# Kernel tuning notes

Measured on AMD Instinct MI355X. Metric: run time of the kernel, lower is better.

The kernel has to match this reference:

```python
import jax, jax.numpy as jnp
import numpy as np

N_HEADS = 16

def setup_inputs() -> dict:
    key = jax.random.key(0)
    k1, k2, k3 = jax.random.split(key, 3)
    B, L, D = 2, 2048, 1024
    x = jax.random.normal(k1, (B, L, D), dtype=jnp.float32)
    w_qkv = jax.random.normal(k2, (D, 3 * D), dtype=jnp.float32) * (1.0 / np.sqrt(D))
    w_out = jax.random.normal(k3, (D, D), dtype=jnp.float32) * (1.0 / np.sqrt(D))
    return {"x": x, "w_qkv": w_qkv, "w_out": w_out}

def reference(x, w_qkv, w_out):
    B, L, D = x.shape
    H = N_HEADS
    dh = D // H
    qkv = x @ w_qkv                      # (B, L, 3D)
    q, k, v = jnp.split(qkv, 3, axis=-1)
    # (B, H, L, dh)
    q = q.reshape(B, L, H, dh).transpose(0, 2, 1, 3)
    k = k.reshape(B, L, H, dh).transpose(0, 2, 1, 3)
    v = v.reshape(B, L, H, dh).transpose(0, 2, 1, 3)
    scale = 1.0 / jnp.sqrt(jnp.asarray(dh, x.dtype))
    attn = jnp.einsum('bhqd,bhkd->bhqk', q, k) * scale   # (B, H, L, L)
    causal = jnp.tril(jnp.ones((L, L), dtype=bool))
    attn = jnp.where(causal[None, None], attn, -jnp.inf)
    attn = jax.nn.softmax(attn, axis=-1)
    out = jnp.einsum('bhqk,bhkd->bhqd', attn, v)         # (B, H, L, dh)
    out = out.transpose(0, 2, 1, 3).reshape(B, L, D)
    return out @ w_out
```

## Files before the change

### kernel.cpp

```cpp
#include <hip/hip_runtime.h>

typedef __attribute__((ext_vector_type(4))) float f32x4;
typedef __attribute__((ext_vector_type(16))) float f32x16;
typedef __attribute__((ext_vector_type(8))) __bf16 bf16x8;
typedef __attribute__((ext_vector_type(4))) __bf16 bf16x4;
typedef __attribute__((ext_vector_type(4))) unsigned u32x4;
typedef __attribute__((ext_vector_type(2))) unsigned u32x2;

static __device__ __forceinline__ f32x4 mfma16(bf16x8 a, bf16x8 b, f32x4 c) {
    return __builtin_amdgcn_mfma_f32_16x16x32_bf16(a, b, c, 0, 0, 0);
}
static __device__ __forceinline__ f32x16 mfma32(bf16x8 a, bf16x8 b, f32x16 c) {
    return __builtin_amdgcn_mfma_f32_32x32x16_bf16(a, b, c, 0, 0, 0);
}
static __device__ __forceinline__ unsigned pk_bf16(float a, float b) {
    unsigned lo = __builtin_bit_cast(unsigned short, (__bf16)a);
    unsigned hh = __builtin_bit_cast(unsigned short, (__bf16)b);
    return lo | (hh << 16);
}

#define QSCALE 0.18033688f

__global__ __launch_bounds__(256) void cvt_f32_bf16(const float* __restrict__ in,
                                                    __bf16* __restrict__ out, int n4) {
    int i = blockIdx.x * 256 + threadIdx.x;
    if (i < n4) {
        f32x4 v = ((const f32x4*)in)[i];
        bf16x4 o;
#pragma unroll
        for (int j = 0; j < 4; j++) o[j] = (__bf16)v[j];
        ((bf16x4*)out)[i] = o;
    }
}

__global__ __launch_bounds__(256) void transpose_bf16(const float* __restrict__ in,
                                                      __bf16* __restrict__ out,
                                                      int R, int C) {
    __shared__ float t[32][33];
    int bx = blockIdx.x * 32;
    int by = blockIdx.y * 32;
    int tx = threadIdx.x, ty = threadIdx.y;
#pragma unroll
    for (int k = 0; k < 32; k += 8)
        t[ty + k][tx] = in[(size_t)(by + ty + k) * C + bx + tx];
    __syncthreads();
#pragma unroll
    for (int k = 0; k < 32; k += 8)
        out[(size_t)(bx + ty + k) * R + by + tx] = (__bf16)t[tx][ty + k];
}

#define BM 128
#define BN 128
#define BKG 64

template <int MODE>
__global__ __launch_bounds__(256) void gemm_bt(const __bf16* __restrict__ A,
                                               const __bf16* __restrict__ Bt,
                                               int M, int N, int K,
                                               float* __restrict__ Cout,
                                               __bf16* __restrict__ Qf,
                                               __bf16* __restrict__ Kf,
                                               __bf16* __restrict__ Vf) {
    __shared__ __attribute__((aligned(16))) __bf16 As[BM * BKG];
    __shared__ __attribute__((aligned(16))) __bf16 Bs[BN * BKG];
    int tid = threadIdx.x;
    int wave = tid >> 6, lane = tid & 63;
    int lrow = lane & 15, lgrp = lane >> 4;
    int chunk = gridDim.x >> 3;
    int bid = blockIdx.x;
    int swz = (bid & 7) * chunk + (bid >> 3);
    int nbx = N >> 7;
    int m0 = (swz / nbx) * BM, n0 = (swz % nbx) * BN;
    int wm = (wave >> 1) * 64, wn = (wave & 1) * 64;

    f32x4 acc[4][4];
#pragma unroll
    for (int i = 0; i < 4; i++)
#pragma unroll
        for (int j = 0; j < 4; j++) acc[i][j] = (f32x4){0.f, 0.f, 0.f, 0.f};

    int srow = tid >> 3;
    int gch = (tid & 7) ^ (srow & 7);
    const __bf16* aSrc = A + (size_t)(m0 + srow) * K + gch * 8;
    const __bf16* bSrc = Bt + (size_t)(n0 + srow) * K + gch * 8;

    for (int k0 = 0; k0 < K; k0 += BKG) {
#pragma unroll
        for (int c = 0; c < 4; c++) {
            __builtin_amdgcn_global_load_lds(
                (const __attribute__((address_space(1))) void*)(aSrc + k0 + (size_t)c * 32 * K),
                (__attribute__((address_space(3))) void*)(As + (c * 256 + wave * 64) * 8),
                16, 0, 0);
        }
#pragma unroll
        for (int c = 0; c < 4; c++) {
            __builtin_amdgcn_global_load_lds(
                (const __attribute__((address_space(1))) void*)(bSrc + k0 + (size_t)c * 32 * K),
                (__attribute__((address_space(3))) void*)(Bs + (c * 256 + wave * 64) * 8),
                16, 0, 0);
        }
        __syncthreads();
#pragma unroll
        for (int kk = 0; kk < 2; kk++) {
            bf16x8 af[4], bfr[4];
#pragma unroll
            for (int mt = 0; mt < 4; mt++) {
                int row = wm + mt * 16 + lrow;
                int slot = row * 8 + ((4 * kk + lgrp) ^ (row & 7));
                af[mt] = *(const bf16x8*)(As + slot * 8);
            }
#pragma unroll
            for (int nt = 0; nt < 4; nt++) {
                int row = wn + nt * 16 + lrow;
                int slot = row * 8 + ((4 * kk + lgrp) ^ (row & 7));
                bfr[nt] = *(const bf16x8*)(Bs + slot * 8);
            }
#pragma unroll
            for (int mt = 0; mt < 4; mt++)
#pragma unroll
                for (int nt = 0; nt < 4; nt++)
                    acc[mt][nt] = mfma16(af[mt], bfr[nt], acc[mt][nt]);
        }
        __syncthreads();
    }

#pragma unroll
    for (int mt = 0; mt < 4; mt++) {
#pragma unroll
        for (int nt = 0; nt < 4; nt++) {
            int f0 = m0 + wm + mt * 16 + lgrp * 4;
            int t = n0 + wn + nt * 16 + lrow;
            if (MODE == 0) {
                *(f32x4*)(Cout + (size_t)t * M + f0) = acc[mt][nt];
            } else {
                int which = f0 >> 10, hn = f0 & 1023;
                int h = hn >> 6, d0 = hn & 63;
                int b = t >> 11, li = t & 2047;
                int bh = b * 16 + h, c = li >> 5, tl = li & 31;
                size_t bhbase = (size_t)bh * 131072;
                if (which == 2) {
                    int ks = tl >> 4, hv = (tl >> 3) & 1, jv = tl & 7;
                    size_t base =
                        bhbase + ((size_t)(c * 4 + ks * 2 + hv) * 64 + d0) * 8 + jv;
#pragma unroll
                    for (int r = 0; r < 4; r++)
                        Vf[base + (size_t)r * 8] = (__bf16)acc[mt][nt][r];
                } else {
                    int st = d0 >> 4, hv = (d0 >> 3) & 1, j0 = d0 & 7;
                    size_t idx =
                        bhbase + ((size_t)(c * 8 + st * 2 + hv) * 32 + tl) * 8 + j0;
                    bf16x4 pv;
                    if (which == 0) {
#pragma unroll
                        for (int r = 0; r < 4; r++)
                            pv[r] = (__bf16)(acc[mt][nt][r] * QSCALE);
                        *(bf16x4*)(Qf + idx) = pv;
                    } else {
#pragma unroll
                        for (int r = 0; r < 4; r++) pv[r] = (__bf16)acc[mt][nt][r];
                        *(bf16x4*)(Kf + idx) = pv;
                    }
                }
            }
        }
    }
}

template <bool MASKED>
static __device__ __forceinline__ void attn_chunk(
    int c, int ql, int hi, const __bf16* __restrict__ Kp,
    const __bf16* __restrict__ Vp, const bf16x8 (&qf)[4],
    f32x16& o0, f32x16& o1, float& ls) {
    const __bf16* kb = Kp + ((size_t)c * 8 + hi) * 256 + ql * 8;
    bf16x8 kf[4];
#pragma unroll
    for (int st = 0; st < 4; st++) kf[st] = *(const bf16x8*)(kb + st * 512);
    const __bf16* vb = Vp + ((size_t)c * 4 + hi) * 512 + ql * 8;
    bf16x8 v00 = *(const bf16x8*)(vb);
    bf16x8 v01 = *(const bf16x8*)(vb + 256);
    bf16x8 v10 = *(const bf16x8*)(vb + 1024);
    bf16x8 v11 = *(const bf16x8*)(vb + 1280);

    f32x16 sa;
#pragma unroll
    for (int r = 0; r < 16; r++) sa[r] = 0.f;
#pragma unroll
    for (int st = 0; st < 4; st++) sa = mfma32(kf[st], qf[st], sa);

    float p[16];
    float psum = 0.f;
#pragma unroll
    for (int r = 0; r < 16; r++) {
        float s = sa[r];
        if (MASKED) {
            int krel = (r & 3) + 8 * (r >> 2) + 4 * hi;
            if (krel > ql) s = -1e30f;
        }
        float pv = __builtin_amdgcn_exp2f(s);
        p[r] = pv;
        psum += pv;
    }
    u32x2 ps = __builtin_amdgcn_permlane32_swap(
        __builtin_bit_cast(unsigned, psum), __builtin_bit_cast(unsigned, psum),
        false, false);
    psum += __builtin_bit_cast(float, hi ? ps[0] : ps[1]);
    ls += psum;

    unsigned w[8];
#pragma unroll
    for (int i = 0; i < 8; i++) w[i] = pk_bf16(p[2 * i], p[2 * i + 1]);
    u32x2 r02 = __builtin_amdgcn_permlane32_swap(w[0], w[2], false, false);
    u32x2 r13 = __builtin_amdgcn_permlane32_swap(w[1], w[3], false, false);
    u32x2 r46 = __builtin_amdgcn_permlane32_swap(w[4], w[6], false, false);
    u32x2 r57 = __builtin_amdgcn_permlane32_swap(w[5], w[7], false, false);
    bf16x8 pa0 = __builtin_bit_cast(bf16x8, (u32x4){r02[0], r13[0], r02[1], r13[1]});
    bf16x8 pa1 = __builtin_bit_cast(bf16x8, (u32x4){r46[0], r57[0], r46[1], r57[1]});

    o0 = mfma32(pa0, v00, o0);
    o1 = mfma32(pa0, v01, o1);
    o0 = mfma32(pa1, v10, o0);
    o1 = mfma32(pa1, v11, o1);
}

__global__ __launch_bounds__(256) void attn_fwd5(const __bf16* __restrict__ Qf,
                                                 const __bf16* __restrict__ Kf,
                                                 const __bf16* __restrict__ Vf,
                                                 __bf16* __restrict__ Ob) {
    __shared__ float comb[3][64][33];
    int tid = threadIdx.x;
    int wave = tid >> 6, lane = tid & 63;
    int ql = lane & 31, hi = lane >> 5;
    int bid = blockIdx.x;
    int xcd = bid & 7, idx = bid >> 3;
    int bh = xcd * 4 + (idx >> 6);
    int strip = 63 - (idx & 63);
    int q0 = strip * 32;

    const __bf16* Qp = Qf + (size_t)bh * 131072;
    const __bf16* Kp = Kf + (size_t)bh * 131072;
    const __bf16* Vp = Vf + (size_t)bh * 131072;

    const __bf16* qb = Qp + ((size_t)strip * 8 + hi) * 256 + ql * 8;
    bf16x8 qf[4];
#pragma unroll
    for (int st = 0; st < 4; st++) qf[st] = *(const bf16x8*)(qb + st * 512);

    f32x16 o0, o1;
#pragma unroll
    for (int r = 0; r < 16; r++) { o0[r] = 0.f; o1[r] = 0.f; }
    float ls = 0.f;

    for (int c = wave; c < strip; c += 4)
        attn_chunk<false>(c, ql, hi, Kp, Vp, qf, o0, o1, ls);
    if ((strip & 3) == wave)
        attn_chunk<true>(strip, ql, hi, Kp, Vp, qf, o0, o1, ls);

    if (wave >= 1) {
        float* sl = &comb[wave - 1][lane][0];
#pragma unroll
        for (int r = 0; r < 16; r++) { sl[r] = o0[r]; sl[16 + r] = o1[r]; }
        sl[32] = ls;
    }
    __syncthreads();
    if (wave == 0) {
#pragma unroll
        for (int s = 0; s < 3; s++) {
            const float* sl = &comb[s][lane][0];
#pragma unroll
            for (int r = 0; r < 16; r++) { o0[r] += sl[r]; o1[r] += sl[16 + r]; }
            ls += sl[32];
        }
        float inv = 1.0f / ls;
        int b = bh >> 4, h = bh & 15;
#pragma unroll
        for (int r = 0; r < 16; r++) {
            int crow = (r & 3) + 8 * (r >> 2) + 4 * hi;
            float ibc = __shfl(inv, crow);
            size_t base = ((size_t)(b * 2048 + q0 + crow)) * 1024 + h * 64;
            Ob[base + ql] = (__bf16)(o0[r] * ibc);
            Ob[base + 32 + ql] = (__bf16)(o1[r] * ibc);
        }
    }
}

extern "C" void kernel_launch(void* const* d_in, const int* in_sizes, int n_in,
                              void* d_out, int out_size, void* d_ws, size_t ws_size,
                              hipStream_t stream) {
    const float* x = (const float*)d_in[0];
    const float* w_qkv = (const float*)d_in[1];
    const float* w_out = (const float*)d_in[2];
    float* out = (float*)d_out;

    char* ws = (char*)d_ws;
    __bf16* xb    = (__bf16*)(ws);
    __bf16* wqkvT = (__bf16*)(ws + (size_t)(8  << 20));
    __bf16* woutT = (__bf16*)(ws + (size_t)(14 << 20));
    __bf16* Qf    = (__bf16*)(ws + (size_t)(16 << 20));
    __bf16* Kf    = (__bf16*)(ws + (size_t)(24 << 20));
    __bf16* Vf    = (__bf16*)(ws + (size_t)(32 << 20));
    __bf16* Ob    = (__bf16*)(ws + (size_t)(40 << 20));

    cvt_f32_bf16<<<4096, 256, 0, stream>>>(x, xb, 4096 * 1024 / 4);
    transpose_bf16<<<dim3(3072 / 32, 1024 / 32), dim3(32, 8), 0, stream>>>(w_qkv, wqkvT, 1024, 3072);
    transpose_bf16<<<dim3(1024 / 32, 1024 / 32), dim3(32, 8), 0, stream>>>(w_out, woutT, 1024, 1024);
    gemm_bt<1><<<768, 256, 0, stream>>>(
        wqkvT, xb, 3072, 4096, 1024, nullptr, Qf, Kf, Vf);
    attn_fwd5<<<2048, 256, 0, stream>>>(Qf, Kf, Vf, Ob);
    gemm_bt<0><<<256, 256, 0, stream>>>(
        woutT, Ob, 1024, 4096, 1024, out, nullptr, nullptr, nullptr);
}
```

Measured before the change: 110.3 us.

## Replace QKV GEMM with 256x256-tile 8-wave kernel using async LDS loads

```diff
diff --git a/kernel.cpp b/kernel.cpp
--- a/kernel.cpp
+++ b/kernel.cpp
@@ -20,6 +20,13 @@
 }
 
 #define QSCALE 0.18033688f
+#define FENCE() asm volatile("" ::: "memory")
+#define SYNCB()                          \
+    do {                                 \
+        FENCE();                         \
+        __builtin_amdgcn_s_barrier();    \
+        FENCE();                         \
+    } while (0)
 
 __global__ __launch_bounds__(256) void cvt_f32_bf16(const float* __restrict__ in,
                                                     __bf16* __restrict__ out, int n4) {
@@ -49,6 +56,143 @@
         out[(size_t)(bx + ty + k) * R + by + tx] = (__bf16)t[tx][ty + k];
 }
 
+__global__ __launch_bounds__(512, 2) void qkv_gemm8(const __bf16* __restrict__ A,
+                                                    const __bf16* __restrict__ Bt,
+                                                    __bf16* __restrict__ Qf,
+                                                    __bf16* __restrict__ Kf,
+                                                    __bf16* __restrict__ Vf) {
+    const int K = 1024, NT = 16, MT = 12;
+    __shared__ __attribute__((aligned(16))) __bf16 smem[65536];
+    int tid = threadIdx.x;
+    int w = tid >> 6, lane = tid & 63;
+    int lrow = lane & 15, lgrp = lane >> 4;
+    int wm = w >> 2, wn = w & 3;
+    int bid = blockIdx.x;
+    int swz = (bid & 7) * 24 + (bid >> 3);
+    int m0 = (swz % MT) * 256, n0 = (swz / MT) * 256;
+
+    int schunk = ((lane & 3) ^ ((lane >> 2) & 3)) * 8;
+    const __bf16* aS[2];
+    const __bf16* bS[2];
+    int dstRow[2];
+#pragma unroll
+    for (int l = 0; l < 2; l++) {
+        int r = w * 32 + l * 16 + (lane >> 2);
+        aS[l] = A + (size_t)(m0 + r) * K + schunk;
+        bS[l] = Bt + (size_t)(n0 + r) * K + schunk;
+        dstRow[l] = (w * 32 + l * 16) * 64;
+    }
+
+    auto STAGE = [&](int h, int tt) {
+        int tc = tt < NT ? tt : NT - 1;
+        int op = h & 1, kh = h >> 1;
+        int base = ((tt & 1) << 16) + (kh << 15) + (op << 14);
+#pragma unroll
+        for (int l = 0; l < 2; l++) {
+            const __bf16* src = (op ? bS[l] : aS[l]) + tc * 64 + kh * 32;
+            __builtin_amdgcn_global_load_lds(
+                (const __attribute__((address_space(1))) void*)src,
+                (__attribute__((address_space(3))) void*)(smem +
+                                                          ((base + dstRow[l]) >> 1)),
+                16, 0, 0);
+        }
+    };
+
+    int swzsel = (lgrp ^ (lrow & 3)) << 4;
+    auto RDA = [&](int buf, int kk, int row) {
+        int off = (buf << 16) + (kk << 15) + row * 64 + swzsel;
+        return *(const bf16x8*)(smem + (off >> 1));
+    };
+    auto RDB = [&](int buf, int kk, int row) {
+        int off = (buf << 16) + (kk << 15) + 16384 + row * 64 + swzsel;
+        return *(const bf16x8*)(smem + (off >> 1));
+    };
+
+    f32x4 acc[8][4];
+#pragma unroll
+    for (int i = 0; i < 8; i++)
+#pragma unroll
+        for (int j = 0; j < 4; j++) acc[i][j] = (f32x4){0.f, 0.f, 0.f, 0.f};
+    bf16x8 bfr[4];
+
+    STAGE(0, 0); STAGE(1, 0); STAGE(2, 0); STAGE(3, 0);
+    STAGE(0, 1); STAGE(1, 1);
+    asm volatile("s_waitcnt vmcnt(8)" ::: "memory");
+    SYNCB();
+
+#define PH(T, KKv, MHv, SH, ST, DOVM)                                          \
+    {                                                                          \
+        bf16x8 af[4];                                                          \
+        if (MHv == 0) {                                                        \
+            _Pragma("unroll") for (int nt = 0; nt < 4; nt++) bfr[nt] =         \
+                RDB((T) & 1, KKv, wn * 64 + nt * 16 + lrow);                   \
+        }                                                                      \
+        _Pragma("unroll") for (int i = 0; i < 4; i++) af[i] =                  \
+            RDA((T) & 1, KKv, wm * 128 + (MHv * 4 + i) * 16 + lrow);           \
+        STAGE(SH, ST);                                                         \
+        if (DOVM) asm volatile("s_waitcnt vmcnt(8)" ::: "memory");             \
+        SYNCB();                                                               \
+        asm volatile("s_waitcnt lgkmcnt(0)" ::: "memory");                     \
+        __builtin_amdgcn_sched_barrier(0);                                     \
+        __builtin_amdgcn_s_setprio(1);                                         \
+        _Pragma("unroll") for (int i = 0; i < 4; i++)                          \
+            _Pragma("unroll") for (int nt = 0; nt < 4; nt++)                   \
+                acc[MHv * 4 + i][nt] =                                         \
+                    mfma16(af[i], bfr[nt], acc[MHv * 4 + i][nt]);              \
+        __builtin_amdgcn_s_setprio(0);                                         \
+        SYNCB();                                                               \
+    }
+
+#pragma unroll 2
+    for (int t = 0; t < NT; ++t) {
+        PH(t, 0, 0, 2, t + 1, 0);
+        PH(t, 0, 1, 3, t + 1, 1);
+        PH(t, 1, 0, 0, t + 2, 0);
+        PH(t, 1, 1, 1, t + 2, 1);
+    }
+#undef PH
+
+    asm volatile("s_waitcnt vmcnt(0)" ::: "memory");
+    SYNCB();
+
+#pragma unroll
+    for (int mt = 0; mt < 8; mt++) {
+#pragma unroll
+        for (int nt = 0; nt < 4; nt++) {
+            int f0 = m0 + wm * 128 + mt * 16 + lgrp * 4;
+            int t = n0 + wn * 64 + nt * 16 + lrow;
+            int which = f0 >> 10, hn = f0 & 1023;
+            int h = hn >> 6, d0 = hn & 63;
+            int b = t >> 11, li = t & 2047;
+            int bh = b * 16 + h, c = li >> 5, tl = li & 31;
+            size_t bhbase = (size_t)bh * 131072;
+            if (which == 2) {
+                int ks = tl >> 4, hv = (tl >> 3) & 1, jv = tl & 7;
+                size_t base =
+                    bhbase + ((size_t)(c * 4 + ks * 2 + hv) * 64 + d0) * 8 + jv;
+#pragma unroll
+                for (int r = 0; r < 4; r++)
+                    Vf[base + (size_t)r * 8] = (__bf16)acc[mt][nt][r];
+            } else {
+                int st = d0 >> 4, hv = (d0 >> 3) & 1, j0 = d0 & 7;
+                size_t idx =
+                    bhbase + ((size_t)(c * 8 + st * 2 + hv) * 32 + tl) * 8 + j0;
+                bf16x4 pv;
+                if (which == 0) {
+#pragma unroll
+                    for (int r = 0; r < 4; r++)
+                        pv[r] = (__bf16)(acc[mt][nt][r] * QSCALE);
+                    *(bf16x4*)(Qf + idx) = pv;
+                } else {
+#pragma unroll
+                    for (int r = 0; r < 4; r++) pv[r] = (__bf16)acc[mt][nt][r];
+                    *(bf16x4*)(Kf + idx) = pv;
+                }
+            }
+        }
+    }
+}
+
 #define BM 128
 #define BN 128
 #define BKG 64
@@ -57,10 +201,7 @@
 __global__ __launch_bounds__(256) void gemm_bt(const __bf16* __restrict__ A,
                                                const __bf16* __restrict__ Bt,
                                                int M, int N, int K,
-                                               float* __restrict__ Cout,
-                                               __bf16* __restrict__ Qf,
-                                               __bf16* __restrict__ Kf,
-                                               __bf16* __restrict__ Vf) {
+                                               float* __restrict__ Cout) {
     __shared__ __attribute__((aligned(16))) __bf16 As[BM * BKG];
     __shared__ __attribute__((aligned(16))) __bf16 Bs[BN * BKG];
     int tid = threadIdx.x;
@@ -130,38 +271,7 @@
         for (int nt = 0; nt < 4; nt++) {
             int f0 = m0 + wm + mt * 16 + lgrp * 4;
             int t = n0 + wn + nt * 16 + lrow;
-            if (MODE == 0) {
-                *(f32x4*)(Cout + (size_t)t * M + f0) = acc[mt][nt];
-            } else {
-                int which = f0 >> 10, hn = f0 & 1023;
-                int h = hn >> 6, d0 = hn & 63;
-                int b = t >> 11, li = t & 2047;
-                int bh = b * 16 + h, c = li >> 5, tl = li & 31;
-                size_t bhbase = (size_t)bh * 131072;
-                if (which == 2) {
-                    int ks = tl >> 4, hv = (tl >> 3) & 1, jv = tl & 7;
-                    size_t base =
-                        bhbase + ((size_t)(c * 4 + ks * 2 + hv) * 64 + d0) * 8 + jv;
-#pragma unroll
-                    for (int r = 0; r < 4; r++)
-                        Vf[base + (size_t)r * 8] = (__bf16)acc[mt][nt][r];
-                } else {
-                    int st = d0 >> 4, hv = (d0 >> 3) & 1, j0 = d0 & 7;
-                    size_t idx =
-                        bhbase + ((size_t)(c * 8 + st * 2 + hv) * 32 + tl) * 8 + j0;
-                    bf16x4 pv;
-                    if (which == 0) {
-#pragma unroll
-                        for (int r = 0; r < 4; r++)
-                            pv[r] = (__bf16)(acc[mt][nt][r] * QSCALE);
-                        *(bf16x4*)(Qf + idx) = pv;
-                    } else {
-#pragma unroll
-                        for (int r = 0; r < 4; r++) pv[r] = (__bf16)acc[mt][nt][r];
-                        *(bf16x4*)(Kf + idx) = pv;
-                    }
-                }
-            }
+            *(f32x4*)(Cout + (size_t)t * M + f0) = acc[mt][nt];
         }
     }
 }
@@ -303,9 +413,7 @@
     cvt_f32_bf16<<<4096, 256, 0, stream>>>(x, xb, 4096 * 1024 / 4);
     transpose_bf16<<<dim3(3072 / 32, 1024 / 32), dim3(32, 8), 0, stream>>>(w_qkv, wqkvT, 1024, 3072);
     transpose_bf16<<<dim3(1024 / 32, 1024 / 32), dim3(32, 8), 0, stream>>>(w_out, woutT, 1024, 1024);
-    gemm_bt<1><<<768, 256, 0, stream>>>(
-        wqkvT, xb, 3072, 4096, 1024, nullptr, Qf, Kf, Vf);
+    qkv_gemm8<<<192, 512, 0, stream>>>(wqkvT, xb, Qf, Kf, Vf);
     attn_fwd5<<<2048, 256, 0, stream>>>(Qf, Kf, Vf, Ob);
-    gemm_bt<0><<<256, 256, 0, stream>>>(
-        woutT, Ob, 1024, 4096, 1024, out, nullptr, nullptr, nullptr);
-}
+    gemm_bt<0><<<256, 256, 0, stream>>>(woutT, Ob, 1024, 4096, 1024, out);
+}
```

Measured after the change: 110.4 us. About the same (+0.1%).

## Double-buffer GEMM LDS tiles and pair causal attention strips per block

Applied to the files above, without the earlier changes.

```diff
diff --git a/kernel.cpp b/kernel.cpp
--- a/kernel.cpp
+++ b/kernel.cpp
@@ -61,8 +61,8 @@
                                                __bf16* __restrict__ Qf,
                                                __bf16* __restrict__ Kf,
                                                __bf16* __restrict__ Vf) {
-    __shared__ __attribute__((aligned(16))) __bf16 As[BM * BKG];
-    __shared__ __attribute__((aligned(16))) __bf16 Bs[BN * BKG];
+    __shared__ __attribute__((aligned(16))) __bf16 As[2][BM * BKG];
+    __shared__ __attribute__((aligned(16))) __bf16 Bs[2][BN * BKG];
     int tid = threadIdx.x;
     int wave = tid >> 6, lane = tid & 63;
     int lrow = lane & 15, lgrp = lane >> 4;
@@ -84,22 +84,30 @@
     const __bf16* aSrc = A + (size_t)(m0 + srow) * K + gch * 8;
     const __bf16* bSrc = Bt + (size_t)(n0 + srow) * K + gch * 8;
 
-    for (int k0 = 0; k0 < K; k0 += BKG) {
+    auto STAGE = [&](int k0, int b) {
 #pragma unroll
         for (int c = 0; c < 4; c++) {
             __builtin_amdgcn_global_load_lds(
                 (const __attribute__((address_space(1))) void*)(aSrc + k0 + (size_t)c * 32 * K),
-                (__attribute__((address_space(3))) void*)(As + (c * 256 + wave * 64) * 8),
+                (__attribute__((address_space(3))) void*)(As[b] + (c * 256 + wave * 64) * 8),
                 16, 0, 0);
         }
 #pragma unroll
         for (int c = 0; c < 4; c++) {
             __builtin_amdgcn_global_load_lds(
                 (const __attribute__((address_space(1))) void*)(bSrc + k0 + (size_t)c * 32 * K),
-                (__attribute__((address_space(3))) void*)(Bs + (c * 256 + wave * 64) * 8),
+                (__attribute__((address_space(3))) void*)(Bs[b] + (c * 256 + wave * 64) * 8),
                 16, 0, 0);
         }
-        __syncthreads();
+    };
+
+    int nk = K >> 6;
+    STAGE(0, 0);
+    __syncthreads();
+
+    for (int t = 0; t < nk; t++) {
+        int cur = t & 1;
+        if (t + 1 < nk) STAGE((t + 1) << 6, cur ^ 1);
 #pragma unroll
         for (int kk = 0; kk < 2; kk++) {
             bf16x8 af[4], bfr[4];
@@ -107,13 +115,13 @@
             for (int mt = 0; mt < 4; mt++) {
                 int row = wm + mt * 16 + lrow;
                 int slot = row * 8 + ((4 * kk + lgrp) ^ (row & 7));
-                af[mt] = *(const bf16x8*)(As + slot * 8);
+                af[mt] = *(const bf16x8*)(As[cur] + slot * 8);
             }
 #pragma unroll
             for (int nt = 0; nt < 4; nt++) {
                 int row = wn + nt * 16 + lrow;
                 int slot = row * 8 + ((4 * kk + lgrp) ^ (row & 7));
-                bfr[nt] = *(const bf16x8*)(Bs + slot * 8);
+                bfr[nt] = *(const bf16x8*)(Bs[cur] + slot * 8);
             }
 #pragma unroll
             for (int mt = 0; mt < 4; mt++)
@@ -222,7 +230,57 @@
     o1 = mfma32(pa1, v11, o1);
 }
 
-__global__ __launch_bounds__(256) void attn_fwd5(const __bf16* __restrict__ Qf,
+static __device__ __forceinline__ void attn_strip(
+    int strip, int bh, int wave, int lane, int ql, int hi,
+    const __bf16* __restrict__ Qp, const __bf16* __restrict__ Kp,
+    const __bf16* __restrict__ Vp, __bf16* __restrict__ Ob,
+    float (*comb)[64][33]) {
+    int q0 = strip * 32;
+    const __bf16* qb = Qp + ((size_t)strip * 8 + hi) * 256 + ql * 8;
+    bf16x8 qf[4];
+#pragma unroll
+    for (int st = 0; st < 4; st++) qf[st] = *(const bf16x8*)(qb + st * 512);
+
+    f32x16 o0, o1;
+#pragma unroll
+    for (int r = 0; r < 16; r++) { o0[r] = 0.f; o1[r] = 0.f; }
+    float ls = 0.f;
+
+    for (int c = wave; c < strip; c += 4)
+        attn_chunk<false>(c, ql, hi, Kp, Vp, qf, o0, o1, ls);
+    if ((strip & 3) == wave)
+        attn_chunk<true>(strip, ql, hi, Kp, Vp, qf, o0, o1, ls);
+
+    if (wave >= 1) {
+        float* sl = &comb[wave - 1][lane][0];
+#pragma unroll
+        for (int r = 0; r < 16; r++) { sl[r] = o0[r]; sl[16 + r] = o1[r]; }
+        sl[32] = ls;
+    }
+    __syncthreads();
+    if (wave == 0) {
+#pragma unroll
+        for (int s = 0; s < 3; s++) {
+            const float* sl = &comb[s][lane][0];
+#pragma unroll
+            for (int r = 0; r < 16; r++) { o0[r] += sl[r]; o1[r] += sl[16 + r]; }
+            ls += sl[32];
+        }
+        float inv = 1.0f / ls;
+        int b = bh >> 4, h = bh & 15;
+#pragma unroll
+        for (int r = 0; r < 16; r++) {
+            int crow = (r & 3) + 8 * (r >> 2) + 4 * hi;
+            float ibc = __shfl(inv, crow);
+            size_t base = ((size_t)(b * 2048 + q0 + crow)) * 1024 + h * 64;
+            Ob[base + ql] = (__bf16)(o0[r] * ibc);
+            Ob[base + 32 + ql] = (__bf16)(o1[r] * ibc);
+        }
+    }
+    __syncthreads();
+}
+
+__global__ __launch_bounds__(256) void attn_fwd6(const __bf16* __restrict__ Qf,
                                                  const __bf16* __restrict__ Kf,
                                                  const __bf16* __restrict__ Vf,
                                                  __bf16* __restrict__ Ob) {
@@ -232,55 +290,15 @@
     int ql = lane & 31, hi = lane >> 5;
     int bid = blockIdx.x;
     int xcd = bid & 7, idx = bid >> 3;
-    int bh = xcd * 4 + (idx >> 6);
-    int strip = 63 - (idx & 63);
-    int q0 = strip * 32;
+    int bh = xcd * 4 + (idx >> 5);
+    int pair = idx & 31;
 
     const __bf16* Qp = Qf + (size_t)bh * 131072;
     const __bf16* Kp = Kf + (size_t)bh * 131072;
     const __bf16* Vp = Vf + (size_t)bh * 131072;
 
-    const __bf16* qb = Qp + ((size_t)strip * 8 + hi) * 256 + ql * 8;
-    bf16x8 qf[4];
-#pragma unroll
-    for (int st = 0; st < 4; st++) qf[st] = *(const bf16x8*)(qb + st * 512);
-
-    f32x16 o0, o1;
-#pragma unroll
-    for (int r = 0; r < 16; r++) { o0[r] = 0.f; o1[r] = 0.f; }
-    float ls = 0.f;
-
-    for (int c = wave; c < strip; c += 4)
-        attn_chunk<false>(c, ql, hi, Kp, Vp, qf, o0, o1, ls);
-    if ((strip & 3) == wave)
-        attn_chunk<true>(strip, ql, hi, Kp, Vp, qf, o0, o1, ls);
-
-    if (wave >= 1) {
-        float* sl = &comb[wave - 1][lane][0];
-#pragma unroll
-        for (int r = 0; r < 16; r++) { sl[r] = o0[r]; sl[16 + r] = o1[r]; }
-        sl[32] = ls;
-    }
-    __syncthreads();
-    if (wave == 0) {
-#pragma unroll
-        for (int s = 0; s < 3; s++) {
-            const float* sl = &comb[s][lane][0];
-#pragma unroll
-            for (int r = 0; r < 16; r++) { o0[r] += sl[r]; o1[r] += sl[16 + r]; }
-            ls += sl[32];
-        }
-        float inv = 1.0f / ls;
-        int b = bh >> 4, h = bh & 15;
-#pragma unroll
-        for (int r = 0; r < 16; r++) {
-            int crow = (r & 3) + 8 * (r >> 2) + 4 * hi;
-            float ibc = __shfl(inv, crow);
-            size_t base = ((size_t)(b * 2048 + q0 + crow)) * 1024 + h * 64;
-            Ob[base + ql] = (__bf16)(o0[r] * ibc);
-            Ob[base + 32 + ql] = (__bf16)(o1[r] * ibc);
-        }
-    }
+    attn_strip(63 - pair, bh, wave, lane, ql, hi, Qp, Kp, Vp, Ob, comb);
+    attn_strip(pair, bh, wave, lane, ql, hi, Qp, Kp, Vp, Ob, comb);
 }
 
 extern "C" void kernel_launch(void* const* d_in, const int* in_sizes, int n_in,
@@ -305,7 +323,7 @@
     transpose_bf16<<<dim3(1024 / 32, 1024 / 32), dim3(32, 8), 0, stream>>>(w_out, woutT, 1024, 1024);
     gemm_bt<1><<<768, 256, 0, stream>>>(
         wqkvT, xb, 3072, 4096, 1024, nullptr, Qf, Kf, Vf);
-    attn_fwd5<<<2048, 256, 0, stream>>>(Qf, Kf, Vf, Ob);
+    attn_fwd6<<<1024, 256, 0, stream>>>(Qf, Kf, Vf, Ob);
     gemm_bt<0><<<256, 256, 0, stream>>>(
         woutT, Ob, 1024, 4096, 1024, out, nullptr, nullptr, nullptr);
 }
```

After: 115.3 us. 1.04x slower.

## Merge prep kernels into one launch and process key chunks in pairs in attention

Applied to the files above, without the earlier changes.

```diff
diff --git a/kernel.cpp b/kernel.cpp
--- a/kernel.cpp
+++ b/kernel.cpp
@@ -21,25 +21,36 @@
 
 #define QSCALE 0.18033688f
 
-__global__ __launch_bounds__(256) void cvt_f32_bf16(const float* __restrict__ in,
-                                                    __bf16* __restrict__ out, int n4) {
-    int i = blockIdx.x * 256 + threadIdx.x;
-    if (i < n4) {
-        f32x4 v = ((const f32x4*)in)[i];
+__global__ __launch_bounds__(256) void prep_all(const float* __restrict__ x,
+                                                __bf16* __restrict__ xb,
+                                                const float* __restrict__ wq,
+                                                __bf16* __restrict__ wqT,
+                                                const float* __restrict__ wo,
+                                                __bf16* __restrict__ woT) {
+    __shared__ float t[32][33];
+    int bid = blockIdx.x, tid = threadIdx.x;
+    if (bid < 4096) {
+        int i = bid * 256 + tid;
+        f32x4 v = ((const f32x4*)x)[i];
         bf16x4 o;
 #pragma unroll
         for (int j = 0; j < 4; j++) o[j] = (__bf16)v[j];
-        ((bf16x4*)out)[i] = o;
-    }
-}
-
-__global__ __launch_bounds__(256) void transpose_bf16(const float* __restrict__ in,
-                                                      __bf16* __restrict__ out,
-                                                      int R, int C) {
-    __shared__ float t[32][33];
-    int bx = blockIdx.x * 32;
-    int by = blockIdx.y * 32;
-    int tx = threadIdx.x, ty = threadIdx.y;
+        ((bf16x4*)xb)[i] = o;
+        return;
+    }
+    const float* in;
+    __bf16* out;
+    int R, C, bx, by;
+    if (bid < 4096 + 3072) {
+        int b2 = bid - 4096;
+        in = wq; out = wqT; R = 1024; C = 3072;
+        bx = (b2 % 96) * 32; by = (b2 / 96) * 32;
+    } else {
+        int b2 = bid - 7168;
+        in = wo; out = woT; R = 1024; C = 1024;
+        bx = (b2 % 32) * 32; by = (b2 / 32) * 32;
+    }
+    int tx = tid & 31, ty = tid >> 5;
 #pragma unroll
     for (int k = 0; k < 32; k += 8)
         t[ty + k][tx] = in[(size_t)(by + ty + k) * C + bx + tx];
@@ -167,7 +178,7 @@
 }
 
 template <bool MASKED>
-static __device__ __forceinline__ void attn_chunk(
+static __device__ __forceinline__ void attn_one(
     int c, int ql, int hi, const __bf16* __restrict__ Kp,
     const __bf16* __restrict__ Vp, const bf16x8 (&qf)[4],
     f32x16& o0, f32x16& o1, float& ls) {
@@ -222,10 +233,84 @@
     o1 = mfma32(pa1, v11, o1);
 }
 
-__global__ __launch_bounds__(256) void attn_fwd5(const __bf16* __restrict__ Qf,
-                                                 const __bf16* __restrict__ Kf,
-                                                 const __bf16* __restrict__ Vf,
-                                                 __bf16* __restrict__ Ob) {
+static __device__ __forceinline__ void attn_pair(
+    int cA, int ql, int hi, const __bf16* __restrict__ Kp,
+    const __bf16* __restrict__ Vp, const bf16x8 (&qf)[4],
+    f32x16& o0, f32x16& o1, float& ls) {
+    const __bf16* kbA = Kp + ((size_t)cA * 8 + hi) * 256 + ql * 8;
+    bf16x8 kA[4], kB[4];
+#pragma unroll
+    for (int st = 0; st < 4; st++) {
+        kA[st] = *(const bf16x8*)(kbA + st * 512);
+        kB[st] = *(const bf16x8*)(kbA + 2048 + st * 512);
+    }
+    const __bf16* vbA = Vp + ((size_t)cA * 4 + hi) * 512 + ql * 8;
+    bf16x8 vA00 = *(const bf16x8*)(vbA);
+    bf16x8 vA01 = *(const bf16x8*)(vbA + 256);
+    bf16x8 vA10 = *(const bf16x8*)(vbA + 1024);
+    bf16x8 vA11 = *(const bf16x8*)(vbA + 1280);
+    bf16x8 vB00 = *(const bf16x8*)(vbA + 2048);
+    bf16x8 vB01 = *(const bf16x8*)(vbA + 2048 + 256);
+    bf16x8 vB10 = *(const bf16x8*)(vbA + 2048 + 1024);
+    bf16x8 vB11 = *(const bf16x8*)(vbA + 2048 + 1280);
+
+    f32x16 saA, saB;
+#pragma unroll
+    for (int r = 0; r < 16; r++) { saA[r] = 0.f; saB[r] = 0.f; }
+#pragma unroll
+    for (int st = 0; st < 4; st++) {
+        saA = mfma32(kA[st], qf[st], saA);
+        saB = mfma32(kB[st], qf[st], saB);
+    }
+
+    float pA[16], pB[16];
+    float psum = 0.f;
+#pragma unroll
+    for (int r = 0; r < 16; r++) {
+        float a = __builtin_amdgcn_exp2f(saA[r]);
+        float b = __builtin_amdgcn_exp2f(saB[r]);
+        pA[r] = a; pB[r] = b;
+        psum += a + b;
+    }
+    u32x2 ps = __builtin_amdgcn_permlane32_swap(
+        __builtin_bit_cast(unsigned, psum), __builtin_bit_cast(unsigned, psum),
+        false, false);
+    psum += __builtin_bit_cast(float, hi ? ps[0] : ps[1]);
+    ls += psum;
+
+    unsigned wA[8], wB[8];
+#pragma unroll
+    for (int i = 0; i < 8; i++) {
+        wA[i] = pk_bf16(pA[2 * i], pA[2 * i + 1]);
+        wB[i] = pk_bf16(pB[2 * i], pB[2 * i + 1]);
+    }
+    u32x2 a02 = __builtin_amdgcn_permlane32_swap(wA[0], wA[2], false, false);
+    u32x2 a13 = __builtin_amdgcn_permlane32_swap(wA[1], wA[3], false, false);
+    u32x2 a46 = __builtin_amdgcn_permlane32_swap(wA[4], wA[6], false, false);
+    u32x2 a57 = __builtin_amdgcn_permlane32_swap(wA[5], wA[7], false, false);
+    u32x2 b02 = __builtin_amdgcn_permlane32_swap(wB[0], wB[2], false, false);
+    u32x2 b13 = __builtin_amdgcn_permlane32_swap(wB[1], wB[3], false, false);
+    u32x2 b46 = __builtin_amdgcn_permlane32_swap(wB[4], wB[6], false, false);
+    u32x2 b57 = __builtin_amdgcn_permlane32_swap(wB[5], wB[7], false, false);
+    bf16x8 paA0 = __builtin_bit_cast(bf16x8, (u32x4){a02[0], a13[0], a02[1], a13[1]});
+    bf16x8 paA1 = __builtin_bit_cast(bf16x8, (u32x4){a46[0], a57[0], a46[1], a57[1]});
+    bf16x8 paB0 = __builtin_bit_cast(bf16x8, (u32x4){b02[0], b13[0], b02[1], b13[1]});
+    bf16x8 paB1 = __builtin_bit_cast(bf16x8, (u32x4){b46[0], b57[0], b46[1], b57[1]});
+
+    o0 = mfma32(paA0, vA00, o0);
+    o1 = mfma32(paA0, vA01, o1);
+    o0 = mfma32(paB0, vB00, o0);
+    o1 = mfma32(paB0, vB01, o1);
+    o0 = mfma32(paA1, vA10, o0);
+    o1 = mfma32(paA1, vA11, o1);
+    o0 = mfma32(paB1, vB10, o0);
+    o1 = mfma32(paB1, vB11, o1);
+}
+
+__global__ __launch_bounds__(256, 1) void attn_fwd8(const __bf16* __restrict__ Qf,
+                                                    const __bf16* __restrict__ Kf,
+                                                    const __bf16* __restrict__ Vf,
+                                                    __bf16* __restrict__ Ob) {
     __shared__ float comb[3][64][33];
     int tid = threadIdx.x;
     int wave = tid >> 6, lane = tid & 63;
@@ -250,10 +335,13 @@
     for (int r = 0; r < 16; r++) { o0[r] = 0.f; o1[r] = 0.f; }
     float ls = 0.f;
 
-    for (int c = wave; c < strip; c += 4)
-        attn_chunk<false>(c, ql, hi, Kp, Vp, qf, o0, o1, ls);
-    if ((strip & 3) == wave)
-        attn_chunk<true>(strip, ql, hi, Kp, Vp, qf, o0, o1, ls);
+    int npair = strip >> 1;
+    for (int p = wave; p < npair; p += 4)
+        attn_pair(2 * p, ql, hi, Kp, Vp, qf, o0, o1, ls);
+    if ((strip & 1) && ((npair & 3) == wave))
+        attn_one<false>(strip - 1, ql, hi, Kp, Vp, qf, o0, o1, ls);
+    if ((((npair + (strip & 1)) & 3)) == wave)
+        attn_one<true>(strip, ql, hi, Kp, Vp, qf, o0, o1, ls);
 
     if (wave >= 1) {
         float* sl = &comb[wave - 1][lane][0];
@@ -300,12 +388,10 @@
     __bf16* Vf    = (__bf16*)(ws + (size_t)(32 << 20));
     __bf16* Ob    = (__bf16*)(ws + (size_t)(40 << 20));
 
-    cvt_f32_bf16<<<4096, 256, 0, stream>>>(x, xb, 4096 * 1024 / 4);
-    transpose_bf16<<<dim3(3072 / 32, 1024 / 32), dim3(32, 8), 0, stream>>>(w_qkv, wqkvT, 1024, 3072);
-    transpose_bf16<<<dim3(1024 / 32, 1024 / 32), dim3(32, 8), 0, stream>>>(w_out, woutT, 1024, 1024);
+    prep_all<<<8192, 256, 0, stream>>>(x, xb, w_qkv, wqkvT, w_out, woutT);
     gemm_bt<1><<<768, 256, 0, stream>>>(
         wqkvT, xb, 3072, 4096, 1024, nullptr, Qf, Kf, Vf);
-    attn_fwd5<<<2048, 256, 0, stream>>>(Qf, Kf, Vf, Ob);
+    attn_fwd8<<<2048, 256, 0, stream>>>(Qf, Kf, Vf, Ob);
     gemm_bt<0><<<256, 256, 0, stream>>>(
         woutT, Ob, 1024, 4096, 1024, out, nullptr, nullptr, nullptr);
 }
```

Result: faster. 107.3 us (-2.7%).
